# Optimization experiments

Measured on AMD Instinct MI355X. Metric: run time of the kernel, lower is better.

The kernel has to match this reference:

```python
import jax, jax.numpy as jnp
import numpy as np

H, W = 16, 16
DIM = 512
HEADS = 8
DIM_HEAD = 64
INNER = HEADS * DIM_HEAD  # 512
B = 8
N = H * W  # 256
SCALE = DIM_HEAD ** -0.5
EPS = 1e-5


def _index_map(h, w):
    # index_map[n, m] = dx * (2w-1) + dy with dx = x-i+h-1, dy = y-j+w-1
    xs = np.arange(h)
    ys = np.arange(w)
    dx = xs[:, None] - xs[None, :] + h - 1            # (h, h)
    dy = ys[:, None] - ys[None, :] + w - 1            # (w, w)
    idx = dx[:, None, :, None] * (2 * w - 1) + dy[None, :, None, :]  # (h, w, h, w)
    return idx.reshape(h * w, h * w).astype(np.int32)


def setup_inputs() -> dict:
    key = jax.random.key(0)
    ks = jax.random.split(key, 5)
    x = jax.random.normal(ks[0], (B, N, DIM), dtype=jnp.float32)
    ln_g = jnp.ones((DIM,), jnp.float32)
    ln_b = jnp.zeros((DIM,), jnp.float32)
    w_qkv = jax.random.normal(ks[1], (DIM, 3 * INNER), jnp.float32) * 0.02
    unique_params = jax.random.normal(ks[2], ((2 * H - 1) * (2 * W - 1), INNER), jnp.float32) * 0.02
    w_out = jax.random.normal(ks[3], (INNER, DIM), jnp.float32) * 0.02
    b_out = jnp.zeros((DIM,), jnp.float32)
    idx_map = jnp.asarray(_index_map(H, W))  # (N, N) int32
    return {"x": x, "ln_g": ln_g, "ln_b": ln_b, "w_qkv": w_qkv,
            "unique_params": unique_params, "w_out": w_out, "b_out": b_out,
            "idx_map": idx_map}


def reference(x, ln_g, ln_b, w_qkv, unique_params, w_out, b_out, idx_map):
    b, n, _ = x.shape
    # LayerNorm
    mu = jnp.mean(x, axis=-1, keepdims=True)
    var = jnp.mean(jnp.square(x - mu), axis=-1, keepdims=True)
    xn = (x - mu) * jax.lax.rsqrt(var + EPS) * ln_g + ln_b
    # qkv projection (no bias)
    qkv = xn @ w_qkv                                  # (b, n, 3*inner)
    q, k, v = jnp.split(qkv, 3, axis=-1)
    q = q.reshape(b, n, HEADS, DIM_HEAD)
    k = k.reshape(b, n, HEADS, DIM_HEAD)
    v = v.reshape(b, n, HEADS, DIM_HEAD)
    # attention scores
    dots = jnp.einsum('bnhd,bmhd->bhnm', q, k) * SCALE
    attn = jax.nn.softmax(dots, axis=-1)              # (b, h, n, m)
    # relative-position table: (n, m, h, d)
    rpos = unique_params[idx_map].reshape(n, n, HEADS, DIM_HEAD)
    # out[b,h,n,d] = sum_m attn[b,h,n,m] * (v[b,m,h,d] + rpos[n,m,h,d])
    out = jnp.einsum('bhnm,bmhd->bnhd', attn, v) \
        + jnp.einsum('bhnm,nmhd->bnhd', attn, rpos)
    out = out.reshape(b, n, INNER)
    return out @ w_out + b_out
```

## Files before the change

### kernel.cpp

```cpp
#include <hip/hip_runtime.h>
#include <math.h>

#define NB 8
#define SEQ 256
#define DIMC 512
#define NHEAD 8
#define DHEAD 64
#define SCALEF 0.125f

typedef __attribute__((ext_vector_type(8))) short s16x8;
typedef __attribute__((ext_vector_type(4))) float f32x4;

static __device__ __forceinline__ unsigned short f2bf(float f) {
  union { float f; unsigned u; } c; c.f = f;
  unsigned r = c.u + 0x7FFF + ((c.u >> 16) & 1);
  return (unsigned short)(r >> 16);
}
static __device__ __forceinline__ float bf2f(unsigned short u) {
  union { unsigned u; float f; } c; c.u = ((unsigned)u) << 16;
  return c.f;
}

__global__ __launch_bounds__(256) void tcast_kernel(const float* __restrict__ W,
    unsigned short* __restrict__ WT, int K, int N) {
  const int n0 = blockIdx.x * 64, k0 = blockIdx.y * 64;
  __shared__ float tile[64][65];
  const int t = threadIdx.x;
#pragma unroll
  for (int i = 0; i < 16; ++i) {
    const int idx = i * 256 + t;
    const int kl = idx >> 6, nl = idx & 63;
    tile[kl][nl] = W[(size_t)(k0 + kl) * N + n0 + nl];
  }
  __syncthreads();
#pragma unroll
  for (int i = 0; i < 16; ++i) {
    const int idx = i * 256 + t;
    const int nl = idx >> 6, kl = idx & 63;
    WT[(size_t)(n0 + nl) * K + k0 + kl] = f2bf(tile[kl][nl]);
  }
}

__global__ __launch_bounds__(256) void ln_kernel(const float* __restrict__ x,
    const float* __restrict__ g, const float* __restrict__ bta,
    unsigned short* __restrict__ xnb) {
  const int row = blockIdx.x;
  const int t = threadIdx.x;
  const float2 v = ((const float2*)(x + (size_t)row * DIMC))[t];
  float s = v.x + v.y;
  float q = v.x * v.x + v.y * v.y;
#pragma unroll
  for (int off = 32; off > 0; off >>= 1) {
    s += __shfl_down(s, off);
    q += __shfl_down(q, off);
  }
  __shared__ float sh_s[4], sh_q[4];
  const int wave = t >> 6, lane = t & 63;
  if (lane == 0) { sh_s[wave] = s; sh_q[wave] = q; }
  __syncthreads();
  const float fs = sh_s[0] + sh_s[1] + sh_s[2] + sh_s[3];
  const float fq = sh_q[0] + sh_q[1] + sh_q[2] + sh_q[3];
  const float mean = fs * (1.0f / DIMC);
  const float inv = rsqrtf(fq * (1.0f / DIMC) - mean * mean + 1e-5f);
  const float2 gv = ((const float2*)g)[t];
  const float2 bv = ((const float2*)bta)[t];
  ushort2 o;
  o.x = f2bf((v.x - mean) * inv * gv.x + bv.x);
  o.y = f2bf((v.y - mean) * inv * gv.y + bv.y);
  ((ushort2*)(xnb + (size_t)row * DIMC))[t] = o;
}

template <int BM, int BN, bool BIAS, bool OUTBF>
__global__ __launch_bounds__(256) void mfma_gemm_bt(
    const unsigned short* __restrict__ A, const unsigned short* __restrict__ BT,
    const float* __restrict__ bias, void* __restrict__ Cv,
    int M, int K, int N) {
  constexpr int TR = BM / 32;
  constexpr int TC = BN / 32;
  __shared__ unsigned short As[BM * 32];
  __shared__ unsigned short Bs[BN * 32];
  const int t = threadIdx.x;
  const int wave = t >> 6, lane = t & 63;
  const int wr = wave >> 1, wc = wave & 1;
  const int bm = blockIdx.x * BM, bn = blockIdx.y * BN;

  f32x4 acc[TR][TC] = {};

  const int fr = lane & 15, q = lane >> 4;
  const int kBlocks = K >> 5;
  for (int kb = 0; kb < kBlocks; ++kb) {
    const int k0 = kb << 5;
    __syncthreads();
#pragma unroll
    for (int c = 0; c < BM * 4 / 256; ++c) {
      const int chunk = c * 256 + t;
      const int row = chunk >> 2, j = chunk & 3;
      const s16x8 v = *(const s16x8*)(A + (size_t)(bm + row) * K + k0 + j * 8);
      *(s16x8*)(As + row * 32 + j * 8) = v;
    }
#pragma unroll
    for (int c = 0; c < BN * 4 / 256; ++c) {
      const int chunk = c * 256 + t;
      const int row = chunk >> 2, j = chunk & 3;
      const s16x8 v = *(const s16x8*)(BT + (size_t)(bn + row) * K + k0 + j * 8);
      *(s16x8*)(Bs + row * 32 + j * 8) = v;
    }
    __syncthreads();
    s16x8 af[TR], bfr[TC];
#pragma unroll
    for (int i = 0; i < TR; ++i) {
      const int row = wr * (BM / 2) + i * 16 + fr;
      af[i] = *(const s16x8*)(As + row * 32 + q * 8);
    }
#pragma unroll
    for (int j = 0; j < TC; ++j) {
      const int row = wc * (BN / 2) + j * 16 + fr;
      bfr[j] = *(const s16x8*)(Bs + row * 32 + q * 8);
    }
#pragma unroll
    for (int i = 0; i < TR; ++i)
#pragma unroll
      for (int j = 0; j < TC; ++j)
        acc[i][j] = __builtin_amdgcn_mfma_f32_16x16x32_bf16(af[i], bfr[j],
                                                            acc[i][j], 0, 0, 0);
  }
#pragma unroll
  for (int i = 0; i < TR; ++i) {
#pragma unroll
    for (int j = 0; j < TC; ++j) {
      const int col = bn + wc * (BN / 2) + j * 16 + fr;
      const float bv = BIAS ? bias[col] : 0.0f;
#pragma unroll
      for (int r = 0; r < 4; ++r) {
        const int row = bm + wr * (BM / 2) + i * 16 + q * 4 + r;
        if constexpr (OUTBF) {
          ((unsigned short*)Cv)[(size_t)row * N + col] = f2bf(acc[i][j][r] + bv);
        } else {
          ((float*)Cv)[(size_t)row * N + col] = acc[i][j][r] + bv;
        }
      }
    }
  }
}

#define PSTR 264
#define KSTR 72
__global__ __launch_bounds__(256) void fused_attn_kernel(
    const unsigned short* __restrict__ qkvb, unsigned short* __restrict__ attnb,
    unsigned short* __restrict__ oav) {
  __shared__ unsigned short kv_lds[256 * KSTR];
  __shared__ unsigned short p_lds[64 * PSTR];
  const int bh = blockIdx.y, b = bh >> 3, h = bh & 7;
  const int n0 = blockIdx.x * 64;
  const int t = threadIdx.x, wave = t >> 6, lane = t & 63;
  const int fr = lane & 15, q4 = lane >> 4;

  {
    const int dc = (t & 7) * 8;
#pragma unroll
    for (int p = 0; p < 8; ++p) {
      const int m = p * 32 + (t >> 3);
      const s16x8 v =
          *(const s16x8*)(qkvb + (size_t)(b * SEQ + m) * 1536 + 512 + h * 64 + dc);
      *(s16x8*)(kv_lds + m * KSTR + dc) = v;
    }
  }
  s16x8 qf[2];
  {
    const size_t qrow = (size_t)(b * SEQ + n0 + wave * 16 + fr) * 1536 + h * 64;
#pragma unroll
    for (int ks = 0; ks < 2; ++ks)
      qf[ks] = *(const s16x8*)(qkvb + qrow + ks * 32 + q4 * 8);
  }
  __syncthreads();

  f32x4 s[16];
#pragma unroll
  for (int mt = 0; mt < 16; ++mt) s[mt] = (f32x4){0.f, 0.f, 0.f, 0.f};
#pragma unroll
  for (int ks = 0; ks < 2; ++ks)
#pragma unroll
    for (int mt = 0; mt < 16; ++mt) {
      const s16x8 kf =
          *(const s16x8*)(kv_lds + (mt * 16 + fr) * KSTR + ks * 32 + q4 * 8);
      s[mt] = __builtin_amdgcn_mfma_f32_16x16x32_bf16(qf[ks], kf, s[mt], 0, 0, 0);
    }

  float mx[4] = {-1e30f, -1e30f, -1e30f, -1e30f};
#pragma unroll
  for (int mt = 0; mt < 16; ++mt)
#pragma unroll
    for (int r = 0; r < 4; ++r) {
      s[mt][r] *= SCALEF;
      mx[r] = fmaxf(mx[r], s[mt][r]);
    }
#pragma unroll
  for (int r = 0; r < 4; ++r) {
    mx[r] = fmaxf(mx[r], __shfl_xor(mx[r], 1));
    mx[r] = fmaxf(mx[r], __shfl_xor(mx[r], 2));
    mx[r] = fmaxf(mx[r], __shfl_xor(mx[r], 4));
    mx[r] = fmaxf(mx[r], __shfl_xor(mx[r], 8));
  }
  float sum[4] = {0.f, 0.f, 0.f, 0.f};
#pragma unroll
  for (int mt = 0; mt < 16; ++mt)
#pragma unroll
    for (int r = 0; r < 4; ++r) {
      s[mt][r] = __expf(s[mt][r] - mx[r]);
      sum[r] += s[mt][r];
    }
#pragma unroll
  for (int r = 0; r < 4; ++r) {
    sum[r] += __shfl_xor(sum[r], 1);
    sum[r] += __shfl_xor(sum[r], 2);
    sum[r] += __shfl_xor(sum[r], 4);
    sum[r] += __shfl_xor(sum[r], 8);
  }
  const float inv0 = 1.0f / sum[0], inv1 = 1.0f / sum[1];
  const float inv2 = 1.0f / sum[2], inv3 = 1.0f / sum[3];
  const float invs[4] = {inv0, inv1, inv2, inv3};

  __syncthreads();

  {
    const int nb = wave * 16 + q4 * 4;
#pragma unroll
    for (int mt = 0; mt < 16; ++mt)
#pragma unroll
      for (int r = 0; r < 4; ++r)
        p_lds[(nb + r) * PSTR + mt * 16 + fr] = f2bf(s[mt][r] * invs[r]);
  }
  {
    const int dc = (t & 7) * 8;
#pragma unroll
    for (int p = 0; p < 8; ++p) {
      const int m = p * 32 + (t >> 3);
      const s16x8 v =
          *(const s16x8*)(qkvb + (size_t)(b * SEQ + m) * 1536 + 1024 + h * 64 + dc);
#pragma unroll
      for (int j = 0; j < 8; ++j) kv_lds[(dc + j) * PSTR + m] = v[j];
    }
  }
  __syncthreads();

#pragma unroll
  for (int p = 0; p < 8; ++p) {
    const int idx = p * 256 + t;
    const int row = idx >> 5, mc = (idx & 31) * 8;
    *(s16x8*)(attnb + (size_t)(bh * SEQ + n0 + row) * SEQ + mc) =
        *(const s16x8*)(p_lds + row * PSTR + mc);
  }

  f32x4 o[4];
#pragma unroll
  for (int dt = 0; dt < 4; ++dt) o[dt] = (f32x4){0.f, 0.f, 0.f, 0.f};
#pragma unroll
  for (int ks = 0; ks < 8; ++ks) {
    const s16x8 pf =
        *(const s16x8*)(p_lds + (wave * 16 + fr) * PSTR + ks * 32 + q4 * 8);
#pragma unroll
    for (int dt = 0; dt < 4; ++dt) {
      const s16x8 vf =
          *(const s16x8*)(kv_lds + (dt * 16 + fr) * PSTR + ks * 32 + q4 * 8);
      o[dt] = __builtin_amdgcn_mfma_f32_16x16x32_bf16(pf, vf, o[dt], 0, 0, 0);
    }
  }
#pragma unroll
  for (int dt = 0; dt < 4; ++dt)
#pragma unroll
    for (int r = 0; r < 4; ++r) {
      const int n = n0 + wave * 16 + q4 * 4 + r;
      oav[(size_t)(b * SEQ + n) * DIMC + h * 64 + dt * 16 + fr] = f2bf(o[dt][r]);
    }
}

#define RSTRIDE 280
__global__ __launch_bounds__(256) void rpos_kernel(
    const unsigned short* __restrict__ attnb, const float* __restrict__ up,
    unsigned short* __restrict__ ob) {
  __shared__ float aS[4][8 * RSTRIDE];
  const int t = threadIdx.x;
  const int wave = t >> 6, lane = t & 63;
  const int g = lane >> 4, dg = lane & 15;
  const int pair = blockIdx.x * 4 + wave;
  const int n = pair >> 3, h = pair & 7;
  float* aW = aS[wave];

  const int m4 = lane * 4;
  const int sm4 = m4 + ((m4 >> 6) << 3);
#pragma unroll
  for (int b = 0; b < 8; ++b) {
    const ushort4 v =
        *(const ushort4*)&attnb[(size_t)((b * 8 + h) * SEQ + n) * SEQ + m4];
    float4 f;
    f.x = bf2f(v.x); f.y = bf2f(v.y); f.z = bf2f(v.z); f.w = bf2f(v.w);
    *(float4*)&aW[b * RSTRIDE + sm4] = f;
  }
  __syncthreads();

  const int xn = n >> 4, yn = n & 15;
  float acc[8][4];
#pragma unroll
  for (int b = 0; b < 8; ++b)
#pragma unroll
    for (int j = 0; j < 4; ++j) acc[b][j] = 0.0f;

  const int mbase = g * 64;
  const int sbase = g * 72;
#pragma unroll 4
  for (int mm = 0; mm < 64; ++mm) {
    const int m = mbase + mm;
    const int xm = m >> 4, ym = m & 15;
    const int row = (xn - xm + 15) * 31 + (yn - ym + 15);
    const float4 u = *(const float4*)&up[(size_t)row * DIMC + h * 64 + dg * 4];
    float ab[8];
#pragma unroll
    for (int b = 0; b < 8; ++b) ab[b] = aW[b * RSTRIDE + sbase + mm];
#pragma unroll
    for (int b = 0; b < 8; ++b) {
      acc[b][0] += ab[b] * u.x;
      acc[b][1] += ab[b] * u.y;
      acc[b][2] += ab[b] * u.z;
      acc[b][3] += ab[b] * u.w;
    }
  }
#pragma unroll
  for (int b = 0; b < 8; ++b)
#pragma unroll
    for (int j = 0; j < 4; ++j) {
      float v = acc[b][j];
      v += __shfl_xor(v, 16);
      v += __shfl_xor(v, 32);
      acc[b][j] = v;
    }
#pragma unroll
  for (int k = 0; k < 2; ++k) {
    const int b = g * 2 + k;
    const size_t base = (size_t)(b * SEQ + n) * DIMC + h * 64 + dg * 4;
    ushort4 pv = *(ushort4*)&ob[base];
    ushort4 w;
    w.x = f2bf(bf2f(pv.x) + acc[b][0]);
    w.y = f2bf(bf2f(pv.y) + acc[b][1]);
    w.z = f2bf(bf2f(pv.z) + acc[b][2]);
    w.w = f2bf(bf2f(pv.w) + acc[b][3]);
    *(ushort4*)&ob[base] = w;
  }
}

extern "C" void kernel_launch(void* const* d_in, const int* in_sizes, int n_in,
                              void* d_out, int out_size, void* d_ws,
                              size_t ws_size, hipStream_t stream) {
  const float* x = (const float*)d_in[0];
  const float* ln_g = (const float*)d_in[1];
  const float* ln_b = (const float*)d_in[2];
  const float* w_qkv = (const float*)d_in[3];
  const float* up = (const float*)d_in[4];
  const float* w_out = (const float*)d_in[5];
  const float* b_out = (const float*)d_in[6];
  float* out = (float*)d_out;

  unsigned short* u = (unsigned short*)d_ws;
  unsigned short* qkvb = u;
  unsigned short* attnb = u + 3145728;
  unsigned short* xnb = u + 7340032;
  unsigned short* ob = u + 8388608;
  unsigned short* wqt = u + 9437184;
  unsigned short* wot = u + 10223616;
  if (ws_size < (size_t)10485760 * sizeof(unsigned short)) return;

  tcast_kernel<<<dim3(24, 8), 256, 0, stream>>>(w_qkv, wqt, 512, 1536);
  tcast_kernel<<<dim3(8, 8), 256, 0, stream>>>(w_out, wot, 512, 512);
  ln_kernel<<<2048, 256, 0, stream>>>(x, ln_g, ln_b, xnb);
  mfma_gemm_bt<128, 128, false, true>
      <<<dim3(16, 12), 256, 0, stream>>>(xnb, wqt, nullptr, qkvb, 2048, 512, 1536);
  fused_attn_kernel<<<dim3(4, 64), 256, 0, stream>>>(qkvb, attnb, ob);
  rpos_kernel<<<512, 256, 0, stream>>>(attnb, up, ob);
  mfma_gemm_bt<64, 64, true, false>
      <<<dim3(32, 8), 256, 0, stream>>>(ob, wot, b_out, out, 2048, 512, 512);
}
```

Baseline: 127.9 us.

## Merge prep kernels, use global_load_lds swizzled GEMM, bf16 rpos table

Merges the two weight transpose-casts and the LayerNorm into one prep kernel, which also converts the relative-position table to bf16. This removes two launches and halves the table traffic in rpos_kernel. The GEMM tile loads now go directly from global memory to LDS via global_load_lds, with an XOR swizzle on the 16-byte chunks to avoid bank conflicts. The trade-off is an extra pass over the position table and lower precision for the position parameters.

After: 123.2 us. 1.04x faster.

```diff
diff --git a/kernel.cpp b/kernel.cpp
--- a/kernel.cpp
+++ b/kernel.cpp
@@ -11,6 +11,12 @@
 typedef __attribute__((ext_vector_type(8))) short s16x8;
 typedef __attribute__((ext_vector_type(4))) float f32x4;
 
+typedef __attribute__((address_space(3))) unsigned int lds_u32_t;
+typedef const __attribute__((address_space(1))) unsigned int g_u32_t;
+static __device__ __forceinline__ void gl_lds16(const void* gsrc, void* ldst) {
+  __builtin_amdgcn_global_load_lds((g_u32_t*)gsrc, (lds_u32_t*)ldst, 16, 0, 0);
+}
+
 static __device__ __forceinline__ unsigned short f2bf(float f) {
   union { float f; unsigned u; } c; c.f = f;
   unsigned r = c.u + 0x7FFF + ((c.u >> 16) & 1);
@@ -21,11 +27,9 @@
   return c.f;
 }
 
-__global__ __launch_bounds__(256) void tcast_kernel(const float* __restrict__ W,
-    unsigned short* __restrict__ WT, int K, int N) {
-  const int n0 = blockIdx.x * 64, k0 = blockIdx.y * 64;
-  __shared__ float tile[64][65];
-  const int t = threadIdx.x;
+static __device__ void tcast_body(const float* __restrict__ W,
+    unsigned short* __restrict__ WT, int K, int N, int n0, int k0, int t,
+    float (*tile)[65]) {
 #pragma unroll
   for (int i = 0; i < 16; ++i) {
     const int idx = i * 256 + t;
@@ -41,33 +45,57 @@
   }
 }
 
-__global__ __launch_bounds__(256) void ln_kernel(const float* __restrict__ x,
+__global__ __launch_bounds__(256) void prep_kernel(const float* __restrict__ x,
     const float* __restrict__ g, const float* __restrict__ bta,
-    unsigned short* __restrict__ xnb) {
-  const int row = blockIdx.x;
+    const float* __restrict__ w_qkv, const float* __restrict__ w_out,
+    const float* __restrict__ up, unsigned short* __restrict__ xnb,
+    unsigned short* __restrict__ wqt, unsigned short* __restrict__ wot,
+    unsigned short* __restrict__ upb) {
+  __shared__ float tile[64][65];
+  __shared__ float sh_s[4], sh_q[4];
   const int t = threadIdx.x;
-  const float2 v = ((const float2*)(x + (size_t)row * DIMC))[t];
-  float s = v.x + v.y;
-  float q = v.x * v.x + v.y * v.y;
-#pragma unroll
-  for (int off = 32; off > 0; off >>= 1) {
-    s += __shfl_down(s, off);
-    q += __shfl_down(q, off);
-  }
-  __shared__ float sh_s[4], sh_q[4];
-  const int wave = t >> 6, lane = t & 63;
-  if (lane == 0) { sh_s[wave] = s; sh_q[wave] = q; }
-  __syncthreads();
-  const float fs = sh_s[0] + sh_s[1] + sh_s[2] + sh_s[3];
-  const float fq = sh_q[0] + sh_q[1] + sh_q[2] + sh_q[3];
-  const float mean = fs * (1.0f / DIMC);
-  const float inv = rsqrtf(fq * (1.0f / DIMC) - mean * mean + 1e-5f);
-  const float2 gv = ((const float2*)g)[t];
-  const float2 bv = ((const float2*)bta)[t];
-  ushort2 o;
-  o.x = f2bf((v.x - mean) * inv * gv.x + bv.x);
-  o.y = f2bf((v.y - mean) * inv * gv.y + bv.y);
-  ((ushort2*)(xnb + (size_t)row * DIMC))[t] = o;
+  const int bid = blockIdx.x;
+  if (bid < 192) {
+    tcast_body(w_qkv, wqt, 512, 1536, (bid % 24) * 64, (bid / 24) * 64, t, tile);
+  } else if (bid < 256) {
+    const int b2 = bid - 192;
+    tcast_body(w_out, wot, 512, 512, (b2 % 8) * 64, (b2 / 8) * 64, t, tile);
+  } else if (bid < 497) {
+    const int base = (bid - 256) * 2048 + t * 4;
+#pragma unroll
+    for (int it = 0; it < 2; ++it) {
+      const int i = base + it * 1024;
+      if (i < 492032) {
+        const float4 v = *(const float4*)&up[i];
+        ushort4 w;
+        w.x = f2bf(v.x); w.y = f2bf(v.y); w.z = f2bf(v.z); w.w = f2bf(v.w);
+        *(ushort4*)&upb[i] = w;
+      }
+    }
+  } else {
+    const int row = bid - 497;
+    const float2 v = ((const float2*)(x + (size_t)row * DIMC))[t];
+    float s = v.x + v.y;
+    float q = v.x * v.x + v.y * v.y;
+#pragma unroll
+    for (int off = 32; off > 0; off >>= 1) {
+      s += __shfl_down(s, off);
+      q += __shfl_down(q, off);
+    }
+    const int wave = t >> 6, lane = t & 63;
+    if (lane == 0) { sh_s[wave] = s; sh_q[wave] = q; }
+    __syncthreads();
+    const float fs = sh_s[0] + sh_s[1] + sh_s[2] + sh_s[3];
+    const float fq = sh_q[0] + sh_q[1] + sh_q[2] + sh_q[3];
+    const float mean = fs * (1.0f / DIMC);
+    const float inv = rsqrtf(fq * (1.0f / DIMC) - mean * mean + 1e-5f);
+    const float2 gv = ((const float2*)g)[t];
+    const float2 bv = ((const float2*)bta)[t];
+    ushort2 o;
+    o.x = f2bf((v.x - mean) * inv * gv.x + bv.x);
+    o.y = f2bf((v.y - mean) * inv * gv.y + bv.y);
+    ((ushort2*)(xnb + (size_t)row * DIMC))[t] = o;
+  }
 }
 
 template <int BM, int BN, bool BIAS, bool OUTBF>
@@ -86,36 +114,40 @@
 
   f32x4 acc[TR][TC] = {};
 
-  const int fr = lane & 15, q = lane >> 4;
+  const int fr = lane & 15, q4 = lane >> 4;
   const int kBlocks = K >> 5;
   for (int kb = 0; kb < kBlocks; ++kb) {
     const int k0 = kb << 5;
     __syncthreads();
 #pragma unroll
     for (int c = 0; c < BM * 4 / 256; ++c) {
-      const int chunk = c * 256 + t;
-      const int row = chunk >> 2, j = chunk & 3;
-      const s16x8 v = *(const s16x8*)(A + (size_t)(bm + row) * K + k0 + j * 8);
-      *(s16x8*)(As + row * 32 + j * 8) = v;
+      const int p = c * 256 + t;
+      const int row = p >> 2;
+      const int jl = (p & 3) ^ ((row >> 1) & 3);
+      gl_lds16(A + (size_t)(bm + row) * K + k0 + jl * 8,
+               As + (size_t)(c * 256 + wave * 64) * 8);
     }
 #pragma unroll
     for (int c = 0; c < BN * 4 / 256; ++c) {
-      const int chunk = c * 256 + t;
-      const int row = chunk >> 2, j = chunk & 3;
-      const s16x8 v = *(const s16x8*)(BT + (size_t)(bn + row) * K + k0 + j * 8);
-      *(s16x8*)(Bs + row * 32 + j * 8) = v;
+      const int p = c * 256 + t;
+      const int row = p >> 2;
+      const int jl = (p & 3) ^ ((row >> 1) & 3);
+      gl_lds16(BT + (size_t)(bn + row) * K + k0 + jl * 8,
+               Bs + (size_t)(c * 256 + wave * 64) * 8);
     }
     __syncthreads();
     s16x8 af[TR], bfr[TC];
 #pragma unroll
     for (int i = 0; i < TR; ++i) {
       const int row = wr * (BM / 2) + i * 16 + fr;
-      af[i] = *(const s16x8*)(As + row * 32 + q * 8);
+      const int jp = q4 ^ ((row >> 1) & 3);
+      af[i] = *(const s16x8*)(As + row * 32 + jp * 8);
     }
 #pragma unroll
     for (int j = 0; j < TC; ++j) {
       const int row = wc * (BN / 2) + j * 16 + fr;
-      bfr[j] = *(const s16x8*)(Bs + row * 32 + q * 8);
+      const int jp = q4 ^ ((row >> 1) & 3);
+      bfr[j] = *(const s16x8*)(Bs + row * 32 + jp * 8);
     }
 #pragma unroll
     for (int i = 0; i < TR; ++i)
@@ -132,7 +164,7 @@
       const float bv = BIAS ? bias[col] : 0.0f;
 #pragma unroll
       for (int r = 0; r < 4; ++r) {
-        const int row = bm + wr * (BM / 2) + i * 16 + q * 4 + r;
+        const int row = bm + wr * (BM / 2) + i * 16 + q4 * 4 + r;
         if constexpr (OUTBF) {
           ((unsigned short*)Cv)[(size_t)row * N + col] = f2bf(acc[i][j][r] + bv);
         } else {
@@ -216,9 +248,8 @@
     sum[r] += __shfl_xor(sum[r], 4);
     sum[r] += __shfl_xor(sum[r], 8);
   }
-  const float inv0 = 1.0f / sum[0], inv1 = 1.0f / sum[1];
-  const float inv2 = 1.0f / sum[2], inv3 = 1.0f / sum[3];
-  const float invs[4] = {inv0, inv1, inv2, inv3};
+  const float invs[4] = {1.0f / sum[0], 1.0f / sum[1], 1.0f / sum[2],
+                         1.0f / sum[3]};
 
   __syncthreads();
 
@@ -276,7 +307,7 @@
 
 #define RSTRIDE 280
 __global__ __launch_bounds__(256) void rpos_kernel(
-    const unsigned short* __restrict__ attnb, const float* __restrict__ up,
+    const unsigned short* __restrict__ attnb, const unsigned short* __restrict__ upb,
     unsigned short* __restrict__ ob) {
   __shared__ float aS[4][8 * RSTRIDE];
   const int t = threadIdx.x;
@@ -312,16 +343,17 @@
     const int m = mbase + mm;
     const int xm = m >> 4, ym = m & 15;
     const int row = (xn - xm + 15) * 31 + (yn - ym + 15);
-    const float4 u = *(const float4*)&up[(size_t)row * DIMC + h * 64 + dg * 4];
+    const ushort4 uu = *(const ushort4*)&upb[(size_t)row * DIMC + h * 64 + dg * 4];
+    const float ux = bf2f(uu.x), uy = bf2f(uu.y), uz = bf2f(uu.z), uw = bf2f(uu.w);
     float ab[8];
 #pragma unroll
     for (int b = 0; b < 8; ++b) ab[b] = aW[b * RSTRIDE + sbase + mm];
 #pragma unroll
     for (int b = 0; b < 8; ++b) {
-      acc[b][0] += ab[b] * u.x;
-      acc[b][1] += ab[b] * u.y;
-      acc[b][2] += ab[b] * u.z;
-      acc[b][3] += ab[b] * u.w;
+      acc[b][0] += ab[b] * ux;
+      acc[b][1] += ab[b] * uy;
+      acc[b][2] += ab[b] * uz;
+      acc[b][3] += ab[b] * uw;
     }
   }
 #pragma unroll
@@ -366,15 +398,15 @@
   unsigned short* ob = u + 8388608;
   unsigned short* wqt = u + 9437184;
   unsigned short* wot = u + 10223616;
-  if (ws_size < (size_t)10485760 * sizeof(unsigned short)) return;
-
-  tcast_kernel<<<dim3(24, 8), 256, 0, stream>>>(w_qkv, wqt, 512, 1536);
-  tcast_kernel<<<dim3(8, 8), 256, 0, stream>>>(w_out, wot, 512, 512);
-  ln_kernel<<<2048, 256, 0, stream>>>(x, ln_g, ln_b, xnb);
+  unsigned short* upb = u + 10485760;
+  if (ws_size < (size_t)10977792 * sizeof(unsigned short)) return;
+
+  prep_kernel<<<2545, 256, 0, stream>>>(x, ln_g, ln_b, w_qkv, w_out, up,
+                                        xnb, wqt, wot, upb);
   mfma_gemm_bt<128, 128, false, true>
       <<<dim3(16, 12), 256, 0, stream>>>(xnb, wqt, nullptr, qkvb, 2048, 512, 1536);
   fused_attn_kernel<<<dim3(4, 64), 256, 0, stream>>>(qkvb, attnb, ob);
-  rpos_kernel<<<512, 256, 0, stream>>>(attnb, up, ob);
+  rpos_kernel<<<512, 256, 0, stream>>>(attnb, upb, ob);
   mfma_gemm_bt<64, 64, true, false>
       <<<dim3(32, 8), 256, 0, stream>>>(ob, wot, b_out, out, 2048, 512, 512);
 }
```
